# Optimization experiments

Hardware: AMD Instinct MI355X
Metric: run time of the kernel (lower is better)

## Reference

```python
import jax, jax.numpy as jnp
import numpy as np

B, CIN, COUT, KH, KW, H, W = 32, 64, 64, 3, 3, 128, 128
STRIDE = (1, 1)
PADDING = [(1, 1), (1, 1)]


def setup_inputs() -> dict:
    key = jax.random.key(0)
    k1, k2, k3, k4 = jax.random.split(key, 4)
    x = jax.random.normal(k1, (B, CIN, H, W), dtype=jnp.float32)
    cov = jax.random.uniform(k2, (B,), dtype=jnp.float32)
    # kaiming-normal fan_out init: std = sqrt(2 / (cout*kh*kw))
    std = np.sqrt(2.0 / (COUT * KH * KW)).astype(np.float32)
    W_0 = jax.random.normal(k3, (COUT, CIN, KH, KW), dtype=jnp.float32) * std
    W_1 = jax.random.normal(k4, (COUT, CIN, KH, KW), dtype=jnp.float32) * std
    return {"x": x, "cov": cov, "W_0": W_0, "W_1": W_1}


def reference(x, cov, W_0, W_1):
    # per-sample kernel: W_0 + cov[i] * W_1  -> [B, COUT, CIN, KH, KW]
    kernels = W_0[None] + cov[:, None, None, None, None] * W_1[None]

    def conv_one(xi, k):
        # xi: [CIN, H, W], k: [COUT, CIN, KH, KW]
        out = jax.lax.conv_general_dilated(
            xi[None], k, window_strides=STRIDE, padding=PADDING,
            dimension_numbers=("NCHW", "OIHW", "NCHW"))
        return out[0]

    return jax.vmap(conv_one)(x, kernels)  # [B, COUT, H, W]
```

## Files before the change

kernel.cpp:

```cpp
#include <hip/hip_runtime.h>
#include <stdint.h>

#define B_   32
#define CIN  64
#define COUT 64
#define H_   128
#define W_   128
#define WP   130

typedef __bf16 bf16x8 __attribute__((ext_vector_type(8)));
typedef float  f32x4  __attribute__((ext_vector_type(4)));

__device__ inline unsigned int f2bf(float f) {
  union { float f; unsigned u; } uf; uf.f = f;
  unsigned u = uf.u;
  unsigned r = 0x7FFFu + ((u >> 16) & 1u);
  return (u + r) >> 16;
}

__device__ inline unsigned int pk2(float a, float b) {
  unsigned short x = __builtin_bit_cast(unsigned short, (__bf16)a);
  unsigned short y = __builtin_bit_cast(unsigned short, (__bf16)b);
  return (unsigned int)x | ((unsigned int)y << 16);
}

__global__ __launch_bounds__(256) void prep_w(const float* __restrict__ W0,
                                              const float* __restrict__ W1,
                                              const float* __restrict__ cov,
                                              unsigned short* __restrict__ Wb) {
  int g  = blockIdx.x * 256 + threadIdx.x;
  int ci = g & 63;
  int co = (g >> 6) & 63;
  int v  = g >> 12;
  int b  = v / 9;
  int p  = v - b * 9;
  int widx = (co * CIN + ci) * 9 + p;
  float val = W0[widx] + cov[b] * W1[widx];
  Wb[g] = (unsigned short)f2bf(val);
}

__global__ __launch_bounds__(512, 4) void conv_fused(
    const float* __restrict__ X,
    const unsigned short* __restrict__ Wb,
    float* __restrict__ out) {
  __shared__ __align__(16) unsigned short Xs[4 * WP * 64];

  int tile = blockIdx.x;
  int b  = tile >> 6;
  int h0 = (tile & 63) * 2;
  int t  = threadIdx.x;
  int wv = t >> 6;
  int l  = t & 63;

  {
    int r    = wv >> 1;
    int half = wv & 1;
    unsigned short* dst_row = Xs + r * (WP * 64);
    unsigned int* d32 = (unsigned int*)(dst_row + half * (129 * 64));
    if (l < 32) d32[l] = 0u;

    int ih = h0 - 1 + r;
    if (ih < 0 || ih > 127) {
      int4 z = {0, 0, 0, 0};
      int4* d = (int4*)(dst_row + 64);
      #pragma unroll
      for (int k = 0; k < 8; k++) d[half * 512 + k * 64 + l] = z;
    } else {
      const int hw = H_ * W_;
      const float* src = X + (((size_t)b * CIN + half * 32) * H_ + ih) * W_ + (l << 1);
      int wp0 = (l << 1) + 1, wp1 = (l << 1) + 2;
      unsigned short* base0 = Xs + r * (WP * 64) + wp0 * 64;
      unsigned short* base1 = Xs + r * (WP * 64) + wp1 * 64;
      int s0 = wp0 & 7, s1 = wp1 & 7;
      #pragma unroll 2
      for (int g = 0; g < 32; g += 4) {
        const float* s = src + (size_t)g * hw;
        float2 a0 = *(const float2*)(s);
        float2 a1 = *(const float2*)(s + hw);
        float2 a2 = *(const float2*)(s + 2 * hw);
        float2 a3 = *(const float2*)(s + 3 * hw);
        uint2 v0, v1;
        v0.x = pk2(a0.x, a1.x); v0.y = pk2(a2.x, a3.x);
        v1.x = pk2(a0.y, a1.y); v1.y = pk2(a2.y, a3.y);
        int ci = half * 32 + g;
        int o = ci >> 3, pos = ci & 7;
        *(uint2*)(base0 + (((o ^ s0) << 3) + pos)) = v0;
        *(uint2*)(base1 + (((o ^ s1) << 3) + pos)) = v1;
      }
    }
  }
  __syncthreads();

  int wvp = wv & 3;
  int wv2 = wv >> 2;
  int lh = l & 15;
  int q  = l >> 4;

  int rbase[4], cbase[4];
  #pragma unroll
  for (int nt = 0; nt < 4; nt++) {
    int p = wvp * 64 + nt * 16 + lh;
    rbase[nt] = p >> 7;
    cbase[nt] = p & 127;
  }

  f32x4 acc[2][4];
  #pragma unroll
  for (int i = 0; i < 2; i++)
    #pragma unroll
    for (int j = 0; j < 4; j++) acc[i][j] = (f32x4){0.f, 0.f, 0.f, 0.f};

  const unsigned short* wbase = Wb + (size_t)b * 9 * 4096 + (size_t)(wv2 * 32) * 64;

  #pragma unroll 1
  for (int kh = 0; kh < 3; kh++) {
    #pragma unroll 1
    for (int kw = 0; kw < 3; kw++) {
      const unsigned short* wk = wbase + (kh * 3 + kw) * 4096;
      #pragma unroll 1
      for (int ck = 0; ck < 2; ck++) {
        bf16x8 af[2], bfr[4];
        #pragma unroll
        for (int mt = 0; mt < 2; mt++)
          af[mt] = *(const bf16x8*)(wk + (mt * 16 + lh) * 64 + ck * 32 + q * 8);
        #pragma unroll
        for (int nt = 0; nt < 4; nt++) {
          int r = rbase[nt] + kh;
          int c = cbase[nt] + kw;
          int blk = (ck * 4 + q) ^ (c & 7);
          bfr[nt] = *(const bf16x8*)(Xs + (r * WP + c) * 64 + blk * 8);
        }
        __builtin_amdgcn_s_setprio(1);
        #pragma unroll
        for (int mt = 0; mt < 2; mt++)
          #pragma unroll
          for (int nt = 0; nt < 4; nt++)
            acc[mt][nt] = __builtin_amdgcn_mfma_f32_16x16x32_bf16(
                af[mt], bfr[nt], acc[mt][nt], 0, 0, 0);
        __builtin_amdgcn_s_setprio(0);
      }
    }
  }

  #pragma unroll
  for (int mt = 0; mt < 2; mt++) {
    int coutb = wv2 * 32 + mt * 16 + q * 4;
    #pragma unroll
    for (int nt = 0; nt < 4; nt++) {
      int oh = h0 + rbase[nt];
      int ow = cbase[nt];
      #pragma unroll
      for (int r = 0; r < 4; r++) {
        int cout = coutb + r;
        out[(((size_t)b * COUT + cout) * H_ + oh) * W_ + ow] = acc[mt][nt][r];
      }
    }
  }
}

extern "C" void kernel_launch(void* const* d_in, const int* in_sizes, int n_in,
                              void* d_out, int out_size, void* d_ws, size_t ws_size,
                              hipStream_t stream) {
  const float* x   = (const float*)d_in[0];
  const float* cov = (const float*)d_in[1];
  const float* W0  = (const float*)d_in[2];
  const float* W1  = (const float*)d_in[3];
  float* out = (float*)d_out;

  unsigned short* Wb = (unsigned short*)d_ws;

  prep_w   <<<dim3(4608), dim3(256), 0, stream>>>(W0, W1, cov, Wb);
  conv_fused<<<dim3(2048), dim3(512), 0, stream>>>(x, Wb, out);
}
```

Baseline: 300.2 us.

## Process 8-row strips per block with rolling 4-row LDS ring and prefetch

Each block now handles an 8-row strip, looping over four 2-row steps. It keeps a 4-slot circular buffer of input rows in shared memory, loading the next two rows into registers while the MFMA work runs and then writing them into LDS. This reuses halo rows across steps instead of reloading four rows for every two output rows, which cuts redundant global reads and bf16 conversion work. In exchange the grid shrinks from 2048 to 512 blocks, which may reduce parallelism, and register pressure rises from the 16 float2 staging registers.

```diff
diff --git a/kernel.cpp b/kernel.cpp
--- a/kernel.cpp
+++ b/kernel.cpp
@@ -7,6 +7,7 @@
 #define H_   128
 #define W_   128
 #define WP   130
+#define HW_  (H_ * W_)
 
 typedef __bf16 bf16x8 __attribute__((ext_vector_type(8)));
 typedef float  f32x4  __attribute__((ext_vector_type(4)));
@@ -39,15 +40,16 @@
   Wb[g] = (unsigned short)f2bf(val);
 }
 
-__global__ __launch_bounds__(512, 4) void conv_fused(
+__global__ __launch_bounds__(512, 4) void conv_strip(
     const float* __restrict__ X,
     const unsigned short* __restrict__ Wb,
     float* __restrict__ out) {
   __shared__ __align__(16) unsigned short Xs[4 * WP * 64];
 
-  int tile = blockIdx.x;
-  int b  = tile >> 6;
-  int h0 = (tile & 63) * 2;
+  int bid   = blockIdx.x;
+  int b     = bid >> 4;
+  int strip = bid & 15;
+  int h0    = strip * 8;
   int t  = threadIdx.x;
   int wv = t >> 6;
   int l  = t & 63;
@@ -60,101 +62,143 @@
     if (l < 32) d32[l] = 0u;
 
     int ih = h0 - 1 + r;
-    if (ih < 0 || ih > 127) {
+    if (ih < 0) {
       int4 z = {0, 0, 0, 0};
       int4* d = (int4*)(dst_row + 64);
       #pragma unroll
-      for (int k = 0; k < 8; k++) d[half * 512 + k * 64 + l] = z;
+      for (int kk = 0; kk < 8; kk++) d[half * 512 + kk * 64 + l] = z;
     } else {
-      const int hw = H_ * W_;
       const float* src = X + (((size_t)b * CIN + half * 32) * H_ + ih) * W_ + (l << 1);
       int wp0 = (l << 1) + 1, wp1 = (l << 1) + 2;
-      unsigned short* base0 = Xs + r * (WP * 64) + wp0 * 64;
-      unsigned short* base1 = Xs + r * (WP * 64) + wp1 * 64;
+      unsigned short* base0 = dst_row + wp0 * 64;
+      unsigned short* base1 = dst_row + wp1 * 64;
       int s0 = wp0 & 7, s1 = wp1 & 7;
       #pragma unroll 2
       for (int g = 0; g < 32; g += 4) {
-        const float* s = src + (size_t)g * hw;
+        const float* s = src + (size_t)g * HW_;
         float2 a0 = *(const float2*)(s);
-        float2 a1 = *(const float2*)(s + hw);
-        float2 a2 = *(const float2*)(s + 2 * hw);
-        float2 a3 = *(const float2*)(s + 3 * hw);
+        float2 a1 = *(const float2*)(s + HW_);
+        float2 a2 = *(const float2*)(s + 2 * HW_);
+        float2 a3 = *(const float2*)(s + 3 * HW_);
         uint2 v0, v1;
         v0.x = pk2(a0.x, a1.x); v0.y = pk2(a2.x, a3.x);
         v1.x = pk2(a0.y, a1.y); v1.y = pk2(a2.y, a3.y);
         int ci = half * 32 + g;
         int o = ci >> 3, pos = ci & 7;
-        *(uint2*)(base0 + (((o ^ s0) << 3) + pos)) = v0;
-        *(uint2*)(base1 + (((o ^ s1) << 3) + pos)) = v1;
+        *(uint2*)(base0 + ((o ^ s0) << 3) + pos) = v0;
+        *(uint2*)(base1 + ((o ^ s1) << 3) + pos) = v1;
       }
     }
   }
-  __syncthreads();
-
-  int wvp = wv & 3;
-  int wv2 = wv >> 2;
+
+  int cq = wv & 3;
+  int a  = wv >> 2;
   int lh = l & 15;
   int q  = l >> 4;
-
   int rbase[4], cbase[4];
   #pragma unroll
   for (int nt = 0; nt < 4; nt++) {
-    int p = wvp * 64 + nt * 16 + lh;
+    int p = cq * 64 + nt * 16 + lh;
     rbase[nt] = p >> 7;
     cbase[nt] = p & 127;
   }
-
-  f32x4 acc[2][4];
-  #pragma unroll
-  for (int i = 0; i < 2; i++)
+  const unsigned short* wbase = Wb + (size_t)b * 9 * 4096 + (size_t)(a * 32) * 64;
+  const float* sbase = X + (((size_t)b * CIN + cq * 16) * H_) * W_ + (l << 1);
+  int wp0 = (l << 1) + 1, wp1 = wp0 + 1;
+  int sw0 = wp0 & 7, sw1 = wp1 & 7;
+
+  __syncthreads();
+
+  #pragma unroll 1
+  for (int k = 0; k < 4; k++) {
+    int h0s = h0 + 2 * k;
+
+    float2 st[16];
+    bool stg = (k < 3);
+    int ih = h0s + 3 + a;
+    if (stg && ih <= 127) {
+      const float* sp = sbase + (size_t)ih * W_;
+      #pragma unroll
+      for (int g = 0; g < 16; g++) st[g] = *(const float2*)(sp + (size_t)g * HW_);
+    } else {
+      #pragma unroll
+      for (int g = 0; g < 16; g++) st[g] = (float2){0.f, 0.f};
+    }
+
+    f32x4 acc[2][4];
     #pragma unroll
-    for (int j = 0; j < 4; j++) acc[i][j] = (f32x4){0.f, 0.f, 0.f, 0.f};
-
-  const unsigned short* wbase = Wb + (size_t)b * 9 * 4096 + (size_t)(wv2 * 32) * 64;
-
-  #pragma unroll 1
-  for (int kh = 0; kh < 3; kh++) {
+    for (int i = 0; i < 2; i++)
+      #pragma unroll
+      for (int j = 0; j < 4; j++) acc[i][j] = (f32x4){0.f, 0.f, 0.f, 0.f};
+
     #pragma unroll 1
-    for (int kw = 0; kw < 3; kw++) {
-      const unsigned short* wk = wbase + (kh * 3 + kw) * 4096;
+    for (int kh = 0; kh < 3; kh++) {
       #pragma unroll 1
-      for (int ck = 0; ck < 2; ck++) {
-        bf16x8 af[2], bfr[4];
+      for (int kw = 0; kw < 3; kw++) {
+        const unsigned short* wk = wbase + (kh * 3 + kw) * 4096;
+        #pragma unroll 1
+        for (int ck = 0; ck < 2; ck++) {
+          bf16x8 af[2], bfr[4];
+          #pragma unroll
+          for (int mt = 0; mt < 2; mt++)
+            af[mt] = *(const bf16x8*)(wk + (mt * 16 + lh) * 64 + ck * 32 + q * 8);
+          #pragma unroll
+          for (int nt = 0; nt < 4; nt++) {
+            int slot = (2 * k + rbase[nt] + kh) & 3;
+            int c = cbase[nt] + kw;
+            int blk = (ck * 4 + q) ^ (c & 7);
+            bfr[nt] = *(const bf16x8*)(Xs + (slot * WP + c) * 64 + blk * 8);
+          }
+          __builtin_amdgcn_s_setprio(1);
+          #pragma unroll
+          for (int mt = 0; mt < 2; mt++)
+            #pragma unroll
+            for (int nt = 0; nt < 4; nt++)
+              acc[mt][nt] = __builtin_amdgcn_mfma_f32_16x16x32_bf16(
+                  af[mt], bfr[nt], acc[mt][nt], 0, 0, 0);
+          __builtin_amdgcn_s_setprio(0);
+        }
+      }
+    }
+
+    __syncthreads();
+
+    if (stg) {
+      int slot = (2 * k + a) & 3;
+      unsigned short* dr = Xs + slot * (WP * 64);
+      #pragma unroll
+      for (int j = 0; j < 2; j++) {
+        int o = cq * 2 + j;
+        uint4 v0, v1;
+        v0.x = pk2(st[j*8+0].x, st[j*8+1].x);
+        v0.y = pk2(st[j*8+2].x, st[j*8+3].x);
+        v0.z = pk2(st[j*8+4].x, st[j*8+5].x);
+        v0.w = pk2(st[j*8+6].x, st[j*8+7].x);
+        v1.x = pk2(st[j*8+0].y, st[j*8+1].y);
+        v1.y = pk2(st[j*8+2].y, st[j*8+3].y);
+        v1.z = pk2(st[j*8+4].y, st[j*8+5].y);
+        v1.w = pk2(st[j*8+6].y, st[j*8+7].y);
+        *(uint4*)(dr + wp0 * 64 + ((o ^ sw0) << 3)) = v0;
+        *(uint4*)(dr + wp1 * 64 + ((o ^ sw1) << 3)) = v1;
+      }
+    }
+
+    #pragma unroll
+    for (int mt = 0; mt < 2; mt++) {
+      int coutb = a * 32 + mt * 16 + q * 4;
+      #pragma unroll
+      for (int nt = 0; nt < 4; nt++) {
+        int oh = h0s + rbase[nt];
+        int ow = cbase[nt];
         #pragma unroll
-        for (int mt = 0; mt < 2; mt++)
-          af[mt] = *(const bf16x8*)(wk + (mt * 16 + lh) * 64 + ck * 32 + q * 8);
-        #pragma unroll
-        for (int nt = 0; nt < 4; nt++) {
-          int r = rbase[nt] + kh;
-          int c = cbase[nt] + kw;
-          int blk = (ck * 4 + q) ^ (c & 7);
-          bfr[nt] = *(const bf16x8*)(Xs + (r * WP + c) * 64 + blk * 8);
+        for (int r = 0; r < 4; r++) {
+          int cout = coutb + r;
+          out[(((size_t)b * COUT + cout) * H_ + oh) * W_ + ow] = acc[mt][nt][r];
         }
-        __builtin_amdgcn_s_setprio(1);
-        #pragma unroll
-        for (int mt = 0; mt < 2; mt++)
-          #pragma unroll
-          for (int nt = 0; nt < 4; nt++)
-            acc[mt][nt] = __builtin_amdgcn_mfma_f32_16x16x32_bf16(
-                af[mt], bfr[nt], acc[mt][nt], 0, 0, 0);
-        __builtin_amdgcn_s_setprio(0);
-      }
-    }
-  }
-
-  #pragma unroll
-  for (int mt = 0; mt < 2; mt++) {
-    int coutb = wv2 * 32 + mt * 16 + q * 4;
-    #pragma unroll
-    for (int nt = 0; nt < 4; nt++) {
-      int oh = h0 + rbase[nt];
-      int ow = cbase[nt];
-      #pragma unroll
-      for (int r = 0; r < 4; r++) {
-        int cout = coutb + r;
-        out[(((size_t)b * COUT + cout) * H_ + oh) * W_ + ow] = acc[mt][nt][r];
-      }
-    }
+      }
+    }
+
+    if (stg) __syncthreads();
   }
 }
 
@@ -169,6 +213,6 @@
 
   unsigned short* Wb = (unsigned short*)d_ws;
 
-  prep_w   <<<dim3(4608), dim3(256), 0, stream>>>(W0, W1, cov, Wb);
-  conv_fused<<<dim3(2048), dim3(512), 0, stream>>>(x, Wb, out);
-}
+  prep_w    <<<dim3(4608), dim3(256), 0, stream>>>(W0, W1, cov, Wb);
+  conv_strip<<<dim3(512),  dim3(512), 0, stream>>>(x, Wb, out);
+}
```

After: 307.2 us. +2.3%, slower.

## Process 16-row strips per block with a rolling LDS row ring buffer

Applied to the files above, without the earlier changes.

Replaces the 2-row tiles with 16-row strips per 1024-thread block. Input rows sit in a 6-slot LDS ring buffer, and the next two rows are prefetched into registers while the current two rows are computed. The conv weights are pre-permuted into an MFMA-fragment order so each A load is a contiguous per-lane read, and block IDs are remapped across batch for L2 locality. This removes the redundant 4-row halo reloads of the old tiling and overlaps global loads with compute. In exchange it launches only 256 blocks (about one per CU) with large registers per thread, and adds a barrier on every step.

```diff
diff --git a/kernel.cpp b/kernel.cpp
--- a/kernel.cpp
+++ b/kernel.cpp
@@ -7,6 +7,8 @@
 #define H_   128
 #define W_   128
 #define WP   130
+#define HW_  (H_ * W_)
+#define SLOT (WP * 64)
 
 typedef __bf16 bf16x8 __attribute__((ext_vector_type(8)));
 typedef float  f32x4  __attribute__((ext_vector_type(4)));
@@ -28,133 +30,154 @@
                                               const float* __restrict__ W1,
                                               const float* __restrict__ cov,
                                               unsigned short* __restrict__ Wb) {
-  int g  = blockIdx.x * 256 + threadIdx.x;
-  int ci = g & 63;
-  int co = (g >> 6) & 63;
-  int v  = g >> 12;
-  int b  = v / 9;
-  int p  = v - b * 9;
-  int widx = (co * CIN + ci) * 9 + p;
+  int g   = blockIdx.x * 256 + threadIdx.x;
+  int j   = g & 7;
+  int l   = (g >> 3) & 63;
+  int cq4 = (g >> 9) & 3;
+  int ck  = (g >> 11) & 1;
+  int v   = g >> 12;
+  int b   = v / 9;
+  int p   = v - b * 9;
+  int cout = cq4 * 16 + (l & 15);
+  int ci   = ck * 32 + (l >> 4) * 8 + j;
+  int widx = (cout * CIN + ci) * 9 + p;
   float val = W0[widx] + cov[b] * W1[widx];
   Wb[g] = (unsigned short)f2bf(val);
 }
 
-__global__ __launch_bounds__(512, 4) void conv_fused(
+__global__ __launch_bounds__(1024, 4) void conv_strip(
     const float* __restrict__ X,
     const unsigned short* __restrict__ Wb,
     float* __restrict__ out) {
-  __shared__ __align__(16) unsigned short Xs[4 * WP * 64];
+  __shared__ __align__(16) unsigned short Xs[6 * SLOT];
 
-  int tile = blockIdx.x;
-  int b  = tile >> 6;
-  int h0 = (tile & 63) * 2;
+  int bid   = blockIdx.x;
+  int b     = (bid & 7) * 4 + (bid >> 6);
+  int strip = (bid >> 3) & 7;
+  int h0    = strip * 16;
+
   int t  = threadIdx.x;
   int wv = t >> 6;
   int l  = t & 63;
+  int lh = l & 15;
+  int q  = l >> 4;
 
+  int a = wv >> 3;
+  int o = wv & 7;
+  int cq4 = wv & 3;
+  int pq  = wv >> 2;
+  int rbase  = pq >> 1;
+  int cbase0 = (pq & 1) * 64 + lh;
+
+  int wp0 = 2 * l + 1, wp1 = 2 * l + 2;
+  int sw0 = (o ^ (wp0 & 7)) << 3, sw1 = (o ^ (wp1 & 7)) << 3;
+
+  if (wv < 6) {
+    unsigned int* d32 = (unsigned int*)(Xs + wv * SLOT + (l < 32 ? 0 : 129 * 64));
+    d32[l & 31] = 0u;
+  }
   {
-    int r    = wv >> 1;
-    int half = wv & 1;
-    unsigned short* dst_row = Xs + r * (WP * 64);
-    unsigned int* d32 = (unsigned int*)(dst_row + half * (129 * 64));
-    if (l < 32) d32[l] = 0u;
-
+    int r  = wv >> 2;
     int ih = h0 - 1 + r;
-    if (ih < 0 || ih > 127) {
-      int4 z = {0, 0, 0, 0};
-      int4* d = (int4*)(dst_row + 64);
-      #pragma unroll
-      for (int k = 0; k < 8; k++) d[half * 512 + k * 64 + l] = z;
-    } else {
-      const int hw = H_ * W_;
-      const float* src = X + (((size_t)b * CIN + half * 32) * H_ + ih) * W_ + (l << 1);
-      int wp0 = (l << 1) + 1, wp1 = (l << 1) + 2;
-      unsigned short* base0 = Xs + r * (WP * 64) + wp0 * 64;
-      unsigned short* base1 = Xs + r * (WP * 64) + wp1 * 64;
-      int s0 = wp0 & 7, s1 = wp1 & 7;
-      #pragma unroll 2
-      for (int g = 0; g < 32; g += 4) {
-        const float* s = src + (size_t)g * hw;
-        float2 a0 = *(const float2*)(s);
-        float2 a1 = *(const float2*)(s + hw);
-        float2 a2 = *(const float2*)(s + 2 * hw);
-        float2 a3 = *(const float2*)(s + 3 * hw);
-        uint2 v0, v1;
-        v0.x = pk2(a0.x, a1.x); v0.y = pk2(a2.x, a3.x);
-        v1.x = pk2(a0.y, a1.y); v1.y = pk2(a2.y, a3.y);
-        int ci = half * 32 + g;
-        int o = ci >> 3, pos = ci & 7;
-        *(uint2*)(base0 + (((o ^ s0) << 3) + pos)) = v0;
-        *(uint2*)(base1 + (((o ^ s1) << 3) + pos)) = v1;
+    unsigned short* dr = Xs + r * SLOT;
+    #pragma unroll
+    for (int oi = 0; oi < 2; oi++) {
+      int oo = (wv & 3) * 2 + oi;
+      uint4 v0 = {0, 0, 0, 0}, v1 = {0, 0, 0, 0};
+      if (ih >= 0) {
+        const float* sp = X + ((size_t)(b * CIN + oo * 8) * H_ + ih) * W_ + 2 * l;
+        float2 tt[8];
+        #pragma unroll
+        for (int j = 0; j < 8; j++) tt[j] = *(const float2*)(sp + (size_t)j * HW_);
+        v0.x = pk2(tt[0].x, tt[1].x); v0.y = pk2(tt[2].x, tt[3].x);
+        v0.z = pk2(tt[4].x, tt[5].x); v0.w = pk2(tt[6].x, tt[7].x);
+        v1.x = pk2(tt[0].y, tt[1].y); v1.y = pk2(tt[2].y, tt[3].y);
+        v1.z = pk2(tt[4].y, tt[5].y); v1.w = pk2(tt[6].y, tt[7].y);
       }
+      *(uint4*)(dr + wp0 * 64 + ((oo ^ (wp0 & 7)) << 3)) = v0;
+      *(uint4*)(dr + wp1 * 64 + ((oo ^ (wp1 & 7)) << 3)) = v1;
     }
   }
   __syncthreads();
 
-  int wvp = wv & 3;
-  int wv2 = wv >> 2;
-  int lh = l & 15;
-  int q  = l >> 4;
+  const unsigned short* wb9 = Wb + (size_t)b * 9 * 4096;
 
-  int rbase[4], cbase[4];
-  #pragma unroll
-  for (int nt = 0; nt < 4; nt++) {
-    int p = wvp * 64 + nt * 16 + lh;
-    rbase[nt] = p >> 7;
-    cbase[nt] = p & 127;
-  }
-
-  f32x4 acc[2][4];
-  #pragma unroll
-  for (int i = 0; i < 2; i++)
-    #pragma unroll
-    for (int j = 0; j < 4; j++) acc[i][j] = (f32x4){0.f, 0.f, 0.f, 0.f};
-
-  const unsigned short* wbase = Wb + (size_t)b * 9 * 4096 + (size_t)(wv2 * 32) * 64;
+  float2 st[8];
+  int sb = 0;
 
   #pragma unroll 1
-  for (int kh = 0; kh < 3; kh++) {
+  for (int k = 0; k < 8; k++) {
+    if (k > 0) {
+      int sw = sb + 2 + a; if (sw >= 6) sw -= 6;
+      unsigned short* dr = Xs + sw * SLOT;
+      uint4 v0, v1;
+      v0.x = pk2(st[0].x, st[1].x); v0.y = pk2(st[2].x, st[3].x);
+      v0.z = pk2(st[4].x, st[5].x); v0.w = pk2(st[6].x, st[7].x);
+      v1.x = pk2(st[0].y, st[1].y); v1.y = pk2(st[2].y, st[3].y);
+      v1.z = pk2(st[4].y, st[5].y); v1.w = pk2(st[6].y, st[7].y);
+      *(uint4*)(dr + wp0 * 64 + sw0) = v0;
+      *(uint4*)(dr + wp1 * 64 + sw1) = v1;
+    }
+    asm volatile("s_waitcnt lgkmcnt(0)" ::: "memory");
+    __builtin_amdgcn_s_barrier();
+    __builtin_amdgcn_sched_barrier(0);
+
+    if (k < 7) {
+      int ih = h0 + 2 * k + 3 + a;
+      if (ih <= 127) {
+        const float* sp = X + ((size_t)(b * CIN + o * 8) * H_ + ih) * W_ + 2 * l;
+        #pragma unroll
+        for (int j = 0; j < 8; j++) st[j] = *(const float2*)(sp + (size_t)j * HW_);
+      } else {
+        #pragma unroll
+        for (int j = 0; j < 8; j++) st[j] = (float2){0.f, 0.f};
+      }
+    }
+    __builtin_amdgcn_sched_barrier(0);
+
+    f32x4 acc[4];
+    #pragma unroll
+    for (int nt = 0; nt < 4; nt++) acc[nt] = (f32x4){0.f, 0.f, 0.f, 0.f};
+
     #pragma unroll 1
-    for (int kw = 0; kw < 3; kw++) {
-      const unsigned short* wk = wbase + (kh * 3 + kw) * 4096;
-      #pragma unroll 1
-      for (int ck = 0; ck < 2; ck++) {
-        bf16x8 af[2], bfr[4];
+    for (int kh = 0; kh < 3; kh++) {
+      int r6 = sb + rbase + kh; if (r6 >= 6) r6 -= 6;
+      const unsigned short* rp = Xs + r6 * SLOT;
+      #pragma unroll
+      for (int kw = 0; kw < 3; kw++) {
+        const unsigned short* wk = wb9 + (kh * 3 + kw) * 4096;
         #pragma unroll
-        for (int mt = 0; mt < 2; mt++)
-          af[mt] = *(const bf16x8*)(wk + (mt * 16 + lh) * 64 + ck * 32 + q * 8);
-        #pragma unroll
-        for (int nt = 0; nt < 4; nt++) {
-          int r = rbase[nt] + kh;
-          int c = cbase[nt] + kw;
-          int blk = (ck * 4 + q) ^ (c & 7);
-          bfr[nt] = *(const bf16x8*)(Xs + (r * WP + c) * 64 + blk * 8);
-        }
-        __builtin_amdgcn_s_setprio(1);
-        #pragma unroll
-        for (int mt = 0; mt < 2; mt++)
+        for (int ck = 0; ck < 2; ck++) {
+          bf16x8 af = *(const bf16x8*)(wk + (ck * 4 + cq4) * 512 + l * 8);
+          bf16x8 bfr[4];
+          #pragma unroll
+          for (int nt = 0; nt < 4; nt++) {
+            int c = cbase0 + nt * 16 + kw;
+            int blk = (ck * 4 + q) ^ (c & 7);
+            bfr[nt] = *(const bf16x8*)(rp + c * 64 + blk * 8);
+          }
+          __builtin_amdgcn_s_setprio(1);
           #pragma unroll
           for (int nt = 0; nt < 4; nt++)
-            acc[mt][nt] = __builtin_amdgcn_mfma_f32_16x16x32_bf16(
-                af[mt], bfr[nt], acc[mt][nt], 0, 0, 0);
-        __builtin_amdgcn_s_setprio(0);
+            acc[nt] = __builtin_amdgcn_mfma_f32_16x16x32_bf16(
+                af, bfr[nt], acc[nt], 0, 0, 0);
+          __builtin_amdgcn_s_setprio(0);
+        }
       }
     }
-  }
 
-  #pragma unroll
-  for (int mt = 0; mt < 2; mt++) {
-    int coutb = wv2 * 32 + mt * 16 + q * 4;
+    int oh = h0 + 2 * k + rbase;
     #pragma unroll
     for (int nt = 0; nt < 4; nt++) {
-      int oh = h0 + rbase[nt];
-      int ow = cbase[nt];
+      int ow = cbase0 + nt * 16;
       #pragma unroll
       for (int r = 0; r < 4; r++) {
-        int cout = coutb + r;
-        out[(((size_t)b * COUT + cout) * H_ + oh) * W_ + ow] = acc[mt][nt][r];
+        int cout = cq4 * 16 + q * 4 + r;
+        out[(((size_t)b * COUT + cout) * H_ + oh) * W_ + ow] = acc[nt][r];
       }
     }
+
+    sb += 2; if (sb >= 6) sb -= 6;
   }
 }
 
@@ -169,6 +192,6 @@
 
   unsigned short* Wb = (unsigned short*)d_ws;
 
-  prep_w   <<<dim3(4608), dim3(256), 0, stream>>>(W0, W1, cov, Wb);
-  conv_fused<<<dim3(2048), dim3(512), 0, stream>>>(x, Wb, out);
+  prep_w    <<<dim3(4608), dim3(256),  0, stream>>>(W0, W1, cov, Wb);
+  conv_strip<<<dim3(256),  dim3(1024), 0, stream>>>(x, Wb, out);
 }
```

Measured after the change: 284.7 us. -5.2%, faster.
